# Kernel tuning notes

Measured on AMD Instinct MI355X. Metric: run time of the kernel, lower is better.

Reference implementation:

```python
import jax, jax.numpy as jnp
import numpy as np

B, S, D, H, L = 8, 512, 1024, 16, 2
DH = D // H
EPS = 1e-6
SCALE = float(np.sqrt(DH))


def _ln(x, g, b):
    # custom LayerNormalization: unbiased std (torch default), eps added to std
    m = x.mean(axis=-1, keepdims=True)
    s = jnp.std(x, axis=-1, keepdims=True, ddof=1)
    return g * (x - m) / (s + EPS) + b


def _pos_encoding(seq_len, dim):
    pos = jnp.arange(seq_len, dtype=jnp.float32)[:, None]
    dims = jnp.arange(dim, dtype=jnp.float32)
    div = 10000.0 ** (2.0 * dims / dim)
    pe = jnp.zeros((seq_len, dim), jnp.float32)
    pe = pe.at[:, 0::2].set(jnp.sin(pos / div[0::2]))
    pe = pe.at[:, 1::2].set(jnp.cos(pos / div[1::2]))
    return pe


def setup_inputs() -> dict:
    key = jax.random.key(0)
    ks = jax.random.split(key, 20)
    std = 0.02
    p = lambda k, shape: jax.random.normal(k, shape, jnp.float32) * std
    return {
        "features": jax.random.normal(ks[0], (B, S, D), jnp.float32),
        "mask": jnp.ones((B, S), jnp.int32),
        "ln_in_g": jnp.ones((D,), jnp.float32),
        "ln_in_b": jnp.zeros((D,), jnp.float32),
        "Wq": p(ks[1], (L, D, D)), "bq": p(ks[2], (L, D)),
        "Wk": p(ks[3], (L, D, D)), "bk": p(ks[4], (L, D)),
        "Wv": p(ks[5], (L, D, D)), "bv": p(ks[6], (L, D)),
        "Wo": p(ks[7], (L, D, D)), "bo": p(ks[8], (L, D)),
        "ln1_g": jnp.ones((L, D), jnp.float32), "ln1_b": jnp.zeros((L, D), jnp.float32),
        "W1": p(ks[9], (L, D, D)), "b1": p(ks[10], (L, D)),
        "W2": p(ks[11], (L, D, D)), "b2": p(ks[12], (L, D)),
        "ln2_g": jnp.ones((L, D), jnp.float32), "ln2_b": jnp.zeros((L, D), jnp.float32),
    }


def reference(features, mask, ln_in_g, ln_in_b, Wq, bq, Wk, bk, Wv, bv, Wo, bo,
              ln1_g, ln1_b, W1, b1, W2, b2, ln2_g, ln2_b):
    # input norm + positional encoding (dropout inert at eval)
    x = _ln(features, ln_in_g, ln_in_b) + _pos_encoding(S, D)  # [B,S,D]
    # mask: positions where mask==0 are masked out with -1e18
    neg = (mask == 0)[:, None, None, :]  # [B,1,1,Sk]

    def encoder_layer(inp, i):
        q = (inp @ Wq[i].T + bq[i]).reshape(B, S, H, DH).transpose(0, 2, 1, 3)
        k = (inp @ Wk[i].T + bk[i]).reshape(B, S, H, DH).transpose(0, 2, 1, 3)
        v = (inp @ Wv[i].T + bv[i]).reshape(B, S, H, DH).transpose(0, 2, 1, 3)
        scores = jnp.einsum('bhqd,bhkd->bhqk', q, k) / SCALE
        scores = jnp.where(neg, -1e18, scores)
        attn = jax.nn.softmax(scores, axis=-1)
        ctx = jnp.einsum('bhqk,bhkd->bhqd', attn, v).transpose(0, 2, 1, 3).reshape(B, S, D)
        attn_out = ctx @ Wo[i].T + bo[i]
        s = _ln(attn_out + inp, ln1_g[i], ln1_b[i])  # residual + custom LN
        h = jax.nn.gelu(s @ W1[i].T + b1[i], approximate=False)
        f = h @ W2[i].T + b2[i]
        return _ln(f + s, ln2_g[i], ln2_b[i])

    # FAITHFUL to source: layers are NOT chained -- each layer reads the
    # original (query,key,value); output is the last layer's result.
    out = x
    for i in range(L):
        out = encoder_layer(x, i)
    return out
```

## Files before the change

kernel.cpp:

```cpp
#include <hip/hip_runtime.h>
#include <cstdint>
#include <cstddef>


typedef __attribute__((ext_vector_type(8))) short bf16x8;
typedef __attribute__((ext_vector_type(4))) short bf16x4;
typedef __attribute__((ext_vector_type(4))) float f32x4;

#define MFMA16(a, b, c) __builtin_amdgcn_mfma_f32_16x16x32_bf16((a), (b), (c), 0, 0, 0)

__device__ __forceinline__ unsigned short f2b(float f) {
  union { float f; unsigned int u; } x; x.f = f;
  unsigned int r = x.u + 0x7fffu + ((x.u >> 16) & 1u);
  return (unsigned short)(r >> 16);
}

__device__ __forceinline__ float b2f(unsigned short u) {
  union { unsigned int i; float f; } x;
  x.i = ((unsigned int)u) << 16;
  return x.f;
}

__device__ __forceinline__ void gl_lds16(const void* g, void* l) {
  __builtin_amdgcn_global_load_lds(
      (const __attribute__((address_space(1))) void*)g,
      (__attribute__((address_space(3))) void*)l, 16, 0, 0);
}

template <int EPI>
__global__ __launch_bounds__(256) void gemm_t(
    const unsigned short* __restrict__ A, const unsigned short* __restrict__ B,
    const float* __restrict__ bias, unsigned short* __restrict__ outB, int N,
    int nnHalf) {
  __shared__ char la[3 * 128 * 128];
  __shared__ char lb[2 * 64 * 128];
  constexpr int K = 1024;
  constexpr int NT = 16;
  const int tid = threadIdx.x;
  const int l = tid & 63, w = tid >> 6;
  const int l15 = l & 15, l4 = l >> 4;
  const int xcd = blockIdx.x & 7, r = blockIdx.x >> 3;
  const int m0 = ((xcd >> 1) * 8 + (r & 7)) * 128;
  const int n0 = ((xcd & 1) * nnHalf + (r >> 3)) * 64;
  const int wr = (w >> 1) * 64, wc = (w & 1) * 32;
  const int sw = l15 & 7;

#define STAGE_A(buf, t)                                                       \
  {                                                                           \
    const int k0_ = (t) * 64;                                                 \
    _Pragma("unroll") for (int i = 0; i < 4; ++i) {                           \
      const int c = i * 256 + tid;                                            \
      const int row = c >> 3;                                                 \
      const int gch = (c & 7) ^ (row & 7);                                    \
      gl_lds16(A + (size_t)(m0 + row) * K + k0_ + gch * 8,                    \
               la + (buf) * 16384 + (i * 256 + w * 64) * 16);                 \
    }                                                                         \
  }
#define STAGE_B(buf, t)                                                       \
  {                                                                           \
    const int k0_ = (t) * 64;                                                 \
    _Pragma("unroll") for (int i = 0; i < 2; ++i) {                           \
      const int c = i * 256 + tid;                                            \
      const int row = c >> 3;                                                 \
      const int gch = (c & 7) ^ (row & 7);                                    \
      gl_lds16(B + (size_t)(n0 + row) * K + k0_ + gch * 8,                    \
               lb + (buf) * 8192 + (i * 256 + w * 64) * 16);                  \
    }                                                                         \
  }

  f32x4 acc[4][2] = {};

  STAGE_A(0, 0);
  STAGE_B(0, 0);
  STAGE_A(1, 1);
  asm volatile("s_waitcnt vmcnt(4)" ::: "memory");
  __builtin_amdgcn_sched_barrier(0);
  __builtin_amdgcn_s_barrier();
  __builtin_amdgcn_sched_barrier(0);

#pragma unroll
  for (int t = 0; t < NT; ++t) {
    if (t + 1 < NT) {
      STAGE_B((t + 1) & 1, t + 1);
    }
    if (t + 2 < NT) {
      STAGE_A((t + 2) % 3, t + 2);
    }
    __builtin_amdgcn_sched_barrier(0);
    const char* abuf = la + (t % 3) * 16384;
    const char* bbuf = lb + (t & 1) * 8192;
#pragma unroll
    for (int kk = 0; kk < 2; ++kk) {
      const unsigned int ch = (unsigned int)(((kk * 4 + l4) ^ sw) << 4);
      bf16x8 af[4], bfr[2];
#pragma unroll
      for (int m = 0; m < 4; ++m)
        af[m] = *(const bf16x8*)(abuf + (wr + m * 16 + l15) * 128 + ch);
#pragma unroll
      for (int n = 0; n < 2; ++n)
        bfr[n] = *(const bf16x8*)(bbuf + (wc + n * 16 + l15) * 128 + ch);
#pragma unroll
      for (int m = 0; m < 4; ++m) {
#pragma unroll
        for (int n = 0; n < 2; ++n) {
          acc[m][n] = MFMA16(af[m], bfr[n], acc[m][n]);
        }
      }
    }
    if (t < NT - 1) {
      if (t + 2 < NT) {
        asm volatile("s_waitcnt vmcnt(4)" ::: "memory");
      } else {
        asm volatile("s_waitcnt vmcnt(0)" ::: "memory");
      }
      __builtin_amdgcn_sched_barrier(0);
      __builtin_amdgcn_s_barrier();
      __builtin_amdgcn_sched_barrier(0);
    }
  }
#undef STAGE_A
#undef STAGE_B

#pragma unroll
  for (int m = 0; m < 4; ++m) {
#pragma unroll
    for (int n = 0; n < 2; ++n) {
      const int col = n0 + wc + n * 16 + l15;
      const float bb = bias[col];
#pragma unroll
      for (int e = 0; e < 4; ++e) {
        const int row = m0 + wr + m * 16 + l4 * 4 + e;
        float v = acc[m][n][e] + bb;
        if (EPI == 1) {
          if (col < 1024) v *= 0.125f;
        } else if (EPI == 2) {
          v = 0.5f * v * (1.f + erff(v * 0.70710678118654752f));
        }
        outB[(size_t)row * N + col] = f2b(v);
      }
    }
  }
}

__global__ __launch_bounds__(256, 2) void attn_kernel(
    const unsigned short* __restrict__ qkv, const int* __restrict__ mask,
    unsigned short* __restrict__ ctx) {
  extern __shared__ char smem[];
  float* maskadd = (float*)(smem + 65536);
  const int bid = blockIdx.x;
  const int b = bid & 7, h = (bid >> 3) & 15, qt = bid >> 7;
  const int tid = threadIdx.x, l = tid & 63, w = tid >> 6;
  const int l15 = l & 15, l4 = l >> 4;
  const size_t RB = (size_t)b * 512 * 3072;

  for (int s = tid; s < 512; s += 256)
    maskadd[s] = mask[b * 512 + s] ? 0.f : -1e18f;

  const unsigned short* Kbase = qkv + RB + 1024 + h * 64;
  const unsigned short* Vbase = qkv + RB + 2048 + h * 64;

  const int kr0 = tid >> 2, kc0 = tid & 3;
  const unsigned int swzk = (unsigned int)((kr0 & 7) << 4);
  const unsigned int ka0 = ((unsigned int)(kr0 * 128 + kc0 * 16)) ^ swzk;
  const unsigned int ka1 = ((unsigned int)(kr0 * 128 + kc0 * 16 + 64)) ^ swzk;
  const int vs0 = 2 * l, vd0 = w * 16;

  bf16x8 k00, k01, k10, k11, vreg[4];
  k00 = *(const bf16x8*)(Kbase + (size_t)kr0 * 3072 + kc0 * 8);
  k01 = *(const bf16x8*)(Kbase + (size_t)kr0 * 3072 + kc0 * 8 + 32);
  k10 = *(const bf16x8*)(Kbase + (size_t)(kr0 + 64) * 3072 + kc0 * 8);
  k11 = *(const bf16x8*)(Kbase + (size_t)(kr0 + 64) * 3072 + kc0 * 8 + 32);
  vreg[0] = *(const bf16x8*)(Vbase + (size_t)vs0 * 3072 + vd0);
  vreg[1] = *(const bf16x8*)(Vbase + (size_t)vs0 * 3072 + vd0 + 8);
  vreg[2] = *(const bf16x8*)(Vbase + (size_t)(vs0 + 1) * 3072 + vd0);
  vreg[3] = *(const bf16x8*)(Vbase + (size_t)(vs0 + 1) * 3072 + vd0 + 8);

  const int q0 = qt * 64 + w * 16;
  const unsigned short* qb =
      qkv + RB + (size_t)(q0 + l15) * 3072 + h * 64 + l4 * 8;
  const bf16x8 qf0 = *(const bf16x8*)(qb);
  const bf16x8 qf1 = *(const bf16x8*)(qb + 32);

#define KWRITE(dst)                        \
  {                                        \
    *(bf16x8*)((dst) + ka0) = k00;         \
    *(bf16x8*)((dst) + ka1) = k01;         \
    *(bf16x8*)((dst) + ka0 + 8192) = k10;  \
    *(bf16x8*)((dst) + ka1 + 8192) = k11;  \
  }
#define VWRITE(dst)                                                          \
  {                                                                          \
    _Pragma("unroll") for (int j = 0; j < 16; ++j) {                         \
      const unsigned short lo_ =                                             \
          (unsigned short)((j < 8) ? vreg[0][j] : vreg[1][j - 8]);           \
      const unsigned short hi_ =                                             \
          (unsigned short)((j < 8) ? vreg[2][j] : vreg[3][j - 8]);           \
      *(unsigned int*)((dst) +                                               \
                       (((vd0 + j) * 256 + vs0 * 2) ^ ((j & 7) << 4))) =     \
          (unsigned int)lo_ | ((unsigned int)hi_ << 16);                     \
    }                                                                        \
  }

  KWRITE(smem);
  VWRITE(smem + 32768);
  __syncthreads();

  const int hi4 = l4 >> 1, gl = l4 & 1, g2 = l4 & 2;
  f32x4 acc[4] = {};
  float run_m = -1e30f, run_s = 0.f;

#pragma unroll
  for (int t = 0; t < 4; ++t) {
    char* kcur = smem + (t & 1) * 16384;
    char* vcur = smem + 32768 + (t & 1) * 16384;
    if (t < 3) {
      const int sn = (t + 1) * 128;
      k00 = *(const bf16x8*)(Kbase + (size_t)(sn + kr0) * 3072 + kc0 * 8);
      k01 = *(const bf16x8*)(Kbase + (size_t)(sn + kr0) * 3072 + kc0 * 8 + 32);
      k10 = *(const bf16x8*)(Kbase + (size_t)(sn + kr0 + 64) * 3072 + kc0 * 8);
      k11 = *(const bf16x8*)(Kbase + (size_t)(sn + kr0 + 64) * 3072 + kc0 * 8 + 32);
      vreg[0] = *(const bf16x8*)(Vbase + (size_t)(sn + vs0) * 3072 + vd0);
      vreg[1] = *(const bf16x8*)(Vbase + (size_t)(sn + vs0) * 3072 + vd0 + 8);
      vreg[2] = *(const bf16x8*)(Vbase + (size_t)(sn + vs0 + 1) * 3072 + vd0);
      vreg[3] = *(const bf16x8*)(Vbase + (size_t)(sn + vs0 + 1) * 3072 + vd0 + 8);
      __builtin_amdgcn_sched_barrier(0);
    }
    f32x4 sc[8];
    __builtin_amdgcn_s_setprio(1);
#pragma unroll
    for (int kk = 0; kk < 8; ++kk) {
      const unsigned int lin = (unsigned int)((kk * 16 + l15) * 128 + l4 * 16);
      const unsigned int swz = (unsigned int)((l15 & 7) << 4);
      const bf16x8 af0 = *(const bf16x8*)(kcur + (lin ^ swz));
      const bf16x8 af1 = *(const bf16x8*)(kcur + ((lin + 64) ^ swz));
      f32x4 c = {0.f, 0.f, 0.f, 0.f};
      c = MFMA16(af0, qf0, c);
      c = MFMA16(af1, qf1, c);
      sc[kk] = c;
    }
    __builtin_amdgcn_s_setprio(0);
    float tmx = -1e30f;
#pragma unroll
    for (int kk = 0; kk < 8; ++kk) {
#pragma unroll
      for (int e = 0; e < 4; ++e) {
        const float v = sc[kk][e] + maskadd[t * 128 + kk * 16 + l4 * 4 + e];
        sc[kk][e] = v;
        tmx = fmaxf(tmx, v);
      }
    }
    tmx = fmaxf(tmx, __shfl_xor(tmx, 16));
    tmx = fmaxf(tmx, __shfl_xor(tmx, 32));
    const float nm = (t == 0) ? tmx : fmaxf(run_m, tmx);
    float tsum = 0.f;
    unsigned int pk[8][2];
#pragma unroll
    for (int kk = 0; kk < 8; ++kk) {
      const float p0 = __expf(sc[kk][0] - nm);
      const float p1 = __expf(sc[kk][1] - nm);
      const float p2 = __expf(sc[kk][2] - nm);
      const float p3 = __expf(sc[kk][3] - nm);
      tsum += (p0 + p1) + (p2 + p3);
      asm("v_cvt_pk_bf16_f32 %0, %1, %2" : "=v"(pk[kk][0]) : "v"(p0), "v"(p1));
      asm("v_cvt_pk_bf16_f32 %0, %1, %2" : "=v"(pk[kk][1]) : "v"(p2), "v"(p3));
    }
    tsum += __shfl_xor(tsum, 16);
    tsum += __shfl_xor(tsum, 32);
    if (t == 0) {
      run_s = tsum;
    } else {
      const float scale = __expf(run_m - nm);
      run_s = run_s * scale + tsum;
      float s4[4];
#pragma unroll
      for (int e = 0; e < 4; ++e) s4[e] = __shfl(scale, l4 * 4 + e);
#pragma unroll
      for (int nt = 0; nt < 4; ++nt) {
#pragma unroll
        for (int e = 0; e < 4; ++e) acc[nt][e] *= s4[e];
      }
    }
    run_m = nm;
#pragma unroll
    for (int k2 = 0; k2 < 4; ++k2) {
      const unsigned int own0 = hi4 ? pk[2 * k2 + 1][0] : pk[2 * k2][0];
      const unsigned int own1 = hi4 ? pk[2 * k2 + 1][1] : pk[2 * k2][1];
      const unsigned int oth0 = hi4 ? pk[2 * k2][0] : pk[2 * k2 + 1][0];
      const unsigned int oth1 = hi4 ? pk[2 * k2][1] : pk[2 * k2 + 1][1];
      const unsigned int s16_0 = (unsigned int)__shfl_xor((int)own0, 16);
      const unsigned int s16_1 = (unsigned int)__shfl_xor((int)own1, 16);
      const unsigned int s32_0 = (unsigned int)__shfl_xor((int)oth0, 32);
      const unsigned int s32_1 = (unsigned int)__shfl_xor((int)oth1, 32);
      const unsigned int s48_0 = (unsigned int)__shfl_xor((int)oth0, 48);
      const unsigned int s48_1 = (unsigned int)__shfl_xor((int)oth1, 48);
      union { unsigned int u[4]; bf16x8 v; } pa;
      pa.u[0] = g2 ? (gl ? s16_0 : s32_0) : (gl ? s48_0 : own0);
      pa.u[1] = g2 ? (gl ? s16_1 : s32_1) : (gl ? s48_1 : own1);
      pa.u[2] = g2 ? (gl ? own0 : s48_0) : (gl ? s32_0 : s16_0);
      pa.u[3] = g2 ? (gl ? own1 : s48_1) : (gl ? s32_1 : s16_1);
      __builtin_amdgcn_s_setprio(1);
#pragma unroll
      for (int nt = 0; nt < 4; ++nt) {
        const int d = nt * 16 + l15;
        const unsigned int vb =
            (unsigned int)((d * 256 + k2 * 64 + l4 * 16) ^ ((l15 & 7) << 4));
        const bf16x8 vbf = *(const bf16x8*)(vcur + vb);
        acc[nt] = MFMA16(pa.v, vbf, acc[nt]);
      }
      __builtin_amdgcn_s_setprio(0);
    }
    if (t < 3) {
      char* knxt = smem + ((t + 1) & 1) * 16384;
      char* vnxt = smem + 32768 + ((t + 1) & 1) * 16384;
      KWRITE(knxt);
      VWRITE(vnxt);
      __syncthreads();
    }
  }
#undef KWRITE
#undef VWRITE

  const float inv = 1.f / run_s;
  float invq[4];
#pragma unroll
  for (int e = 0; e < 4; ++e) invq[e] = __shfl(inv, l4 * 4 + e);
#pragma unroll
  for (int nt = 0; nt < 4; ++nt) {
#pragma unroll
    for (int e = 0; e < 4; ++e) {
      const size_t row = (size_t)b * 512 + q0 + l4 * 4 + e;
      ctx[row * 1024 + h * 64 + nt * 16 + l15] = f2b(acc[nt][e] * invq[e]);
    }
  }
}

template <int MODE>
__global__ __launch_bounds__(256) void ln_k(
    const void* __restrict__ Ap, const void* __restrict__ Rp,
    const float* __restrict__ g, const float* __restrict__ bta,
    void* __restrict__ outp) {
  __shared__ float red[8];
  const int row = blockIdx.x, tid = threadIdx.x;
  const size_t base = (size_t)row * 1024 + tid * 4;
  float a4[4];
  if (MODE == 0) {
    const float4 a = *(const float4*)((const float*)Ap + base);
    a4[0] = a.x; a4[1] = a.y; a4[2] = a.z; a4[3] = a.w;
  } else {
    const bf16x4 a = *(const bf16x4*)((const unsigned short*)Ap + base);
    const bf16x4 rr = *(const bf16x4*)((const unsigned short*)Rp + base);
#pragma unroll
    for (int j = 0; j < 4; ++j)
      a4[j] = b2f((unsigned short)a[j]) + b2f((unsigned short)rr[j]);
  }
  float s = a4[0] + a4[1] + a4[2] + a4[3];
  float q = a4[0] * a4[0] + a4[1] * a4[1] + a4[2] * a4[2] + a4[3] * a4[3];
#pragma unroll
  for (int o = 32; o; o >>= 1) {
    s += __shfl_xor(s, o);
    q += __shfl_xor(q, o);
  }
  if ((tid & 63) == 0) {
    red[(tid >> 6) * 2] = s;
    red[(tid >> 6) * 2 + 1] = q;
  }
  __syncthreads();
  const float S = red[0] + red[2] + red[4] + red[6];
  const float Qs = red[1] + red[3] + red[5] + red[7];
  const float mean = S * (1.f / 1024.f);
  float var = (Qs - 1024.f * mean * mean) * (1.f / 1023.f);
  var = fmaxf(var, 0.f);
  const float inv = 1.f / (sqrtf(var) + 1e-6f);
  float o4[4];
#pragma unroll
  for (int j = 0; j < 4; ++j) {
    const int col = tid * 4 + j;
    float y = g[col] * (a4[j] - mean) * inv + bta[col];
    if (MODE == 0) {
      const float ang =
          (float)(row & 511) * exp2f((float)col * -0.025952563241307518f);
      y += (col & 1) ? cosf(ang) : sinf(ang);
    }
    o4[j] = y;
  }
  if (MODE == 2) {
    *(float4*)((float*)outp + base) = make_float4(o4[0], o4[1], o4[2], o4[3]);
  } else {
    bf16x4 pb;
    pb[0] = (short)f2b(o4[0]);
    pb[1] = (short)f2b(o4[1]);
    pb[2] = (short)f2b(o4[2]);
    pb[3] = (short)f2b(o4[3]);
    *(bf16x4*)((unsigned short*)outp + base) = pb;
  }
}

__global__ __launch_bounds__(256) void prep_weights(
    const float* __restrict__ Wq, const float* __restrict__ Wk,
    const float* __restrict__ Wv, const float* __restrict__ Wo,
    const float* __restrict__ W1, const float* __restrict__ W2,
    const float* __restrict__ bq, const float* __restrict__ bk,
    const float* __restrict__ bv, unsigned short* __restrict__ wqkv,
    unsigned short* __restrict__ wo, unsigned short* __restrict__ w1,
    unsigned short* __restrict__ w2, float* __restrict__ bqkv) {
  const int gid = blockIdx.x * 256 + threadIdx.x;
  if (gid < 1572864) {
    const int chunk = gid >> 18;
    const int off = (gid & 262143) * 4;
    const float* s;
    unsigned short* d;
    switch (chunk) {
      case 0: s = Wq; d = wqkv; break;
      case 1: s = Wk; d = wqkv + 1048576; break;
      case 2: s = Wv; d = wqkv + 2097152; break;
      case 3: s = Wo; d = wo; break;
      case 4: s = W1; d = w1; break;
      default: s = W2; d = w2; break;
    }
    const float4 v = *(const float4*)(s + off);
    bf16x4 o;
    o[0] = (short)f2b(v.x); o[1] = (short)f2b(v.y);
    o[2] = (short)f2b(v.z); o[3] = (short)f2b(v.w);
    *(bf16x4*)(d + off) = o;
  } else {
    const int idx = (gid - 1572864) * 4;
    if (idx < 3072) {
      const float* bs = idx < 1024 ? bq : (idx < 2048 ? bk - 1024 : bv - 2048);
      *(float4*)(bqkv + idx) = *(const float4*)(bs + idx);
    }
  }
}

extern "C" void kernel_launch(void* const* d_in, const int* in_sizes, int n_in,
                              void* d_out, int out_size, void* d_ws, size_t ws_size,
                              hipStream_t stream) {
  (void)in_sizes; (void)n_in; (void)out_size; (void)ws_size;
  const float* features = (const float*)d_in[0];
  const int* mask = (const int*)d_in[1];
  const float* ln_in_g = (const float*)d_in[2];
  const float* ln_in_b = (const float*)d_in[3];
  const size_t DD = 1024 * 1024;
  const float* Wq = (const float*)d_in[4] + DD;
  const float* bq = (const float*)d_in[5] + 1024;
  const float* Wk = (const float*)d_in[6] + DD;
  const float* bk = (const float*)d_in[7] + 1024;
  const float* Wv = (const float*)d_in[8] + DD;
  const float* bv = (const float*)d_in[9] + 1024;
  const float* Wo = (const float*)d_in[10] + DD;
  const float* bo = (const float*)d_in[11] + 1024;
  const float* l1g = (const float*)d_in[12] + 1024;
  const float* l1b = (const float*)d_in[13] + 1024;
  const float* W1 = (const float*)d_in[14] + DD;
  const float* b1 = (const float*)d_in[15] + 1024;
  const float* W2 = (const float*)d_in[16] + DD;
  const float* b2 = (const float*)d_in[17] + 1024;
  const float* l2g = (const float*)d_in[18] + 1024;
  const float* l2b = (const float*)d_in[19] + 1024;

  char* base = (char*)d_ws;
  unsigned short* qkv = (unsigned short*)(base);
  unsigned short* xb = (unsigned short*)(base + 25165824);
  unsigned short* ctxb = (unsigned short*)(base + 33554432);
  unsigned short* abuf = (unsigned short*)(base + 41943040);
  unsigned short* wqkv = (unsigned short*)(base + 50331648);
  unsigned short* wo = (unsigned short*)(base + 56623104);
  unsigned short* w1 = (unsigned short*)(base + 58720256);
  unsigned short* w2 = (unsigned short*)(base + 60817408);
  float* bqkv = (float*)(base + 62914560);

  hipFuncSetAttribute((const void*)attn_kernel,
                      hipFuncAttributeMaxDynamicSharedMemorySize, 67584);

  prep_weights<<<6147, 256, 0, stream>>>(Wq, Wk, Wv, Wo, W1, W2, bq, bk, bv,
                                         wqkv, wo, w1, w2, bqkv);
  ln_k<0><<<4096, 256, 0, stream>>>(features, nullptr, ln_in_g, ln_in_b, xb);
  gemm_t<1><<<1536, 256, 0, stream>>>(xb, wqkv, bqkv, qkv, 3072, 24);
  attn_kernel<<<1024, 256, 67584, stream>>>(qkv, mask, ctxb);
  gemm_t<3><<<512, 256, 0, stream>>>(ctxb, wo, bo, abuf, 1024, 8);
  ln_k<1><<<4096, 256, 0, stream>>>(abuf, xb, l1g, l1b, ctxb);
  gemm_t<2><<<512, 256, 0, stream>>>(ctxb, w1, b1, xb, 1024, 8);
  gemm_t<3><<<512, 256, 0, stream>>>(xb, w2, b2, abuf, 1024, 8);
  ln_k<2><<<4096, 256, 0, stream>>>(abuf, ctxb, l2g, l2b, (float*)d_out);
}
```

Baseline: 158.3 us.

## Add dedicated 128x128-tile QKV GEMM and read attention mask directly

Introduces a separate QKV projection kernel with 128x128 output tiles, a 3-stage LDS pipeline in dynamic shared memory (96KB) and a 4x4 MFMA fragment grid per wave. This halves the grid and raises arithmetic intensity per block compared with the 128x64 generic GEMM. The attention kernel also drops its LDS mask table and instead loads the int mask from global memory as int4 per fragment, shrinking its shared memory footprint. The larger LDS use of the QKV kernel limits how many blocks fit per CU, and the mask loads add global memory traffic inside the softmax loop.

```diff
diff --git a/kernel.cpp b/kernel.cpp
--- a/kernel.cpp
+++ b/kernel.cpp
@@ -27,8 +27,108 @@
       (__attribute__((address_space(3))) void*)l, 16, 0, 0);
 }
 
+__global__ __launch_bounds__(256) void gemm_qkv(
+    const unsigned short* __restrict__ A, const unsigned short* __restrict__ B,
+    const float* __restrict__ bias, unsigned short* __restrict__ outB, int N,
+    int K, int nnHalf) {
+  extern __shared__ char smem[];
+  char* la = smem;
+  char* lb = smem + 3 * 16384;
+  const int tid = threadIdx.x;
+  const int l = tid & 63, w = tid >> 6;
+  const int l15 = l & 15, l4 = l >> 4;
+  const int xcd = blockIdx.x & 7, r = blockIdx.x >> 3;
+  const int m0 = ((xcd >> 1) * 8 + (r & 7)) * 128;
+  const int n0 = ((xcd & 1) * nnHalf + (r >> 3)) * 128;
+  const int wr = (w >> 1) * 64, wc = (w & 1) * 64;
+  const int NT = K >> 6;
+
+#define STAGE(buf, t)                                                         \
+  {                                                                           \
+    const int k0_ = (t) * 64;                                                 \
+    _Pragma("unroll") for (int i = 0; i < 4; ++i) {                           \
+      const int c = i * 256 + tid;                                            \
+      const int row = c >> 3;                                                 \
+      const int gch = (c & 7) ^ (row & 7);                                    \
+      gl_lds16(A + (size_t)(m0 + row) * K + k0_ + gch * 8,                    \
+               la + (buf) * 16384 + (i * 256 + w * 64) * 16);                 \
+    }                                                                         \
+    _Pragma("unroll") for (int i = 0; i < 4; ++i) {                           \
+      const int c = i * 256 + tid;                                            \
+      const int row = c >> 3;                                                 \
+      const int gch = (c & 7) ^ (row & 7);                                    \
+      gl_lds16(B + (size_t)(n0 + row) * K + k0_ + gch * 8,                    \
+               lb + (buf) * 16384 + (i * 256 + w * 64) * 16);                 \
+    }                                                                         \
+  }
+
+  f32x4 acc[4][4] = {};
+  const int sw = l15 & 7;
+
+  STAGE(0, 0);
+  STAGE(1, 1);
+  asm volatile("s_waitcnt vmcnt(8)" ::: "memory");
+  __builtin_amdgcn_sched_barrier(0);
+  __builtin_amdgcn_s_barrier();
+  __builtin_amdgcn_sched_barrier(0);
+
+  for (int t = 0; t < NT; ++t) {
+    if (t + 2 < NT) {
+      STAGE((t + 2) % 3, t + 2);
+    }
+    __builtin_amdgcn_sched_barrier(0);
+    const char* abuf = la + (t % 3) * 16384;
+    const char* bbuf = lb + (t % 3) * 16384;
+#pragma unroll
+    for (int kk = 0; kk < 2; ++kk) {
+      const unsigned int ch = (unsigned int)(((kk * 4 + l4) ^ sw) << 4);
+      bf16x8 af[4], bfr[4];
+#pragma unroll
+      for (int m = 0; m < 4; ++m)
+        af[m] = *(const bf16x8*)(abuf + (wr + m * 16 + l15) * 128 + ch);
+#pragma unroll
+      for (int n = 0; n < 4; ++n)
+        bfr[n] = *(const bf16x8*)(bbuf + (wc + n * 16 + l15) * 128 + ch);
+#pragma unroll
+      for (int m = 0; m < 4; ++m) {
+#pragma unroll
+        for (int n = 0; n < 4; ++n) {
+          acc[m][n] = MFMA16(af[m], bfr[n], acc[m][n]);
+        }
+      }
+    }
+    if (t < NT - 1) {
+      if (t + 2 < NT) {
+        asm volatile("s_waitcnt vmcnt(8)" ::: "memory");
+      } else {
+        asm volatile("s_waitcnt vmcnt(0)" ::: "memory");
+      }
+      __builtin_amdgcn_sched_barrier(0);
+      __builtin_amdgcn_s_barrier();
+      __builtin_amdgcn_sched_barrier(0);
+    }
+  }
+#undef STAGE
+
+#pragma unroll
+  for (int m = 0; m < 4; ++m) {
+#pragma unroll
+    for (int n = 0; n < 4; ++n) {
+      const int col = n0 + wc + n * 16 + l15;
+      const float bb = bias[col];
+#pragma unroll
+      for (int e = 0; e < 4; ++e) {
+        const int row = m0 + wr + m * 16 + l4 * 4 + e;
+        float v = acc[m][n][e] + bb;
+        if (col < 1024) v *= 0.125f;
+        outB[(size_t)row * N + col] = f2b(v);
+      }
+    }
+  }
+}
+
 template <int EPI>
-__global__ __launch_bounds__(256) void gemm_t(
+__global__ __launch_bounds__(256) void gemm_s(
     const unsigned short* __restrict__ A, const unsigned short* __restrict__ B,
     const float* __restrict__ bias, unsigned short* __restrict__ outB, int N,
     int nnHalf) {
@@ -131,9 +231,7 @@
       for (int e = 0; e < 4; ++e) {
         const int row = m0 + wr + m * 16 + l4 * 4 + e;
         float v = acc[m][n][e] + bb;
-        if (EPI == 1) {
-          if (col < 1024) v *= 0.125f;
-        } else if (EPI == 2) {
+        if (EPI == 2) {
           v = 0.5f * v * (1.f + erff(v * 0.70710678118654752f));
         }
         outB[(size_t)row * N + col] = f2b(v);
@@ -146,15 +244,12 @@
     const unsigned short* __restrict__ qkv, const int* __restrict__ mask,
     unsigned short* __restrict__ ctx) {
   extern __shared__ char smem[];
-  float* maskadd = (float*)(smem + 65536);
   const int bid = blockIdx.x;
   const int b = bid & 7, h = (bid >> 3) & 15, qt = bid >> 7;
   const int tid = threadIdx.x, l = tid & 63, w = tid >> 6;
   const int l15 = l & 15, l4 = l >> 4;
   const size_t RB = (size_t)b * 512 * 3072;
-
-  for (int s = tid; s < 512; s += 256)
-    maskadd[s] = mask[b * 512 + s] ? 0.f : -1e18f;
+  const int* mrow = mask + b * 512;
 
   const unsigned short* Kbase = qkv + RB + 1024 + h * 64;
   const unsigned short* Vbase = qkv + RB + 2048 + h * 64;
@@ -242,12 +337,13 @@
     float tmx = -1e30f;
 #pragma unroll
     for (int kk = 0; kk < 8; ++kk) {
-#pragma unroll
-      for (int e = 0; e < 4; ++e) {
-        const float v = sc[kk][e] + maskadd[t * 128 + kk * 16 + l4 * 4 + e];
-        sc[kk][e] = v;
-        tmx = fmaxf(tmx, v);
-      }
+      const int4 mv = *(const int4*)(mrow + t * 128 + kk * 16 + l4 * 4);
+      sc[kk][0] += mv.x ? 0.f : -1e18f;
+      sc[kk][1] += mv.y ? 0.f : -1e18f;
+      sc[kk][2] += mv.z ? 0.f : -1e18f;
+      sc[kk][3] += mv.w ? 0.f : -1e18f;
+#pragma unroll
+      for (int e = 0; e < 4; ++e) tmx = fmaxf(tmx, sc[kk][e]);
     }
     tmx = fmaxf(tmx, __shfl_xor(tmx, 16));
     tmx = fmaxf(tmx, __shfl_xor(tmx, 32));
@@ -468,17 +564,19 @@
   unsigned short* w2 = (unsigned short*)(base + 60817408);
   float* bqkv = (float*)(base + 62914560);
 
+  hipFuncSetAttribute((const void*)gemm_qkv,
+                      hipFuncAttributeMaxDynamicSharedMemorySize, 98304);
   hipFuncSetAttribute((const void*)attn_kernel,
-                      hipFuncAttributeMaxDynamicSharedMemorySize, 67584);
+                      hipFuncAttributeMaxDynamicSharedMemorySize, 65536);
 
   prep_weights<<<6147, 256, 0, stream>>>(Wq, Wk, Wv, Wo, W1, W2, bq, bk, bv,
                                          wqkv, wo, w1, w2, bqkv);
   ln_k<0><<<4096, 256, 0, stream>>>(features, nullptr, ln_in_g, ln_in_b, xb);
-  gemm_t<1><<<1536, 256, 0, stream>>>(xb, wqkv, bqkv, qkv, 3072, 24);
-  attn_kernel<<<1024, 256, 67584, stream>>>(qkv, mask, ctxb);
-  gemm_t<3><<<512, 256, 0, stream>>>(ctxb, wo, bo, abuf, 1024, 8);
+  gemm_qkv<<<768, 256, 98304, stream>>>(xb, wqkv, bqkv, qkv, 3072, 1024, 12);
+  attn_kernel<<<1024, 256, 65536, stream>>>(qkv, mask, ctxb);
+  gemm_s<3><<<512, 256, 0, stream>>>(ctxb, wo, bo, abuf, 1024, 8);
   ln_k<1><<<4096, 256, 0, stream>>>(abuf, xb, l1g, l1b, ctxb);
-  gemm_t<2><<<512, 256, 0, stream>>>(ctxb, w1, b1, xb, 1024, 8);
-  gemm_t<3><<<512, 256, 0, stream>>>(xb, w2, b2, abuf, 1024, 8);
+  gemm_s<2><<<512, 256, 0, stream>>>(ctxb, w1, b1, xb, 1024, 8);
+  gemm_s<3><<<512, 256, 0, stream>>>(xb, w2, b2, abuf, 1024, 8);
   ln_k<2><<<4096, 256, 0, stream>>>(abuf, ctxb, l2g, l2b, (float*)d_out);
 }
```

Measured after the change: 164.3 us. 1.04x slower.
